# Performance work log

Hardware: AMD Instinct MI355X
Metric: run time of the kernel (lower is better)

Reference implementation:

```python
import jax, jax.numpy as jnp
import numpy as np

DIM = 1024
HEADS = 16
DIM_HEAD = 64
INNER = HEADS * DIM_HEAD  # 1024
MLP = 4096
EPS = 1e-5


def layer_norm(x, gamma, beta):
    mu = jnp.mean(x, axis=-1, keepdims=True)
    var = jnp.var(x, axis=-1, keepdims=True)
    return (x - mu) * jax.lax.rsqrt(var + EPS) * gamma + beta


def setup_inputs() -> dict:
    key = jax.random.key(0)
    ks = jax.random.split(key, 10)
    s = 0.02
    return {
        "x": jax.random.normal(ks[0], (2, 2048, DIM), dtype=jnp.float32),
        "ln1_g": jnp.ones((DIM,), jnp.float32),
        "ln1_b": jnp.zeros((DIM,), jnp.float32),
        "w_qkv": jax.random.normal(ks[1], (DIM, 3 * INNER), jnp.float32) * s,
        "w_out": jax.random.normal(ks[2], (INNER, DIM), jnp.float32) * s,
        "b_out": jnp.zeros((DIM,), jnp.float32),
        "ln2_g": jnp.ones((DIM,), jnp.float32),
        "ln2_b": jnp.zeros((DIM,), jnp.float32),
        "w1": jax.random.normal(ks[3], (DIM, MLP), jnp.float32) * s,
        "b1": jnp.zeros((MLP,), jnp.float32),
        "w2": jax.random.normal(ks[4], (MLP, DIM), jnp.float32) * s,
        "b2": jnp.zeros((DIM,), jnp.float32),
    }


def reference(x, ln1_g, ln1_b, w_qkv, w_out, b_out, ln2_g, ln2_b, w1, b1, w2, b2):
    b, n, _ = x.shape
    scale = DIM_HEAD ** -0.5

    # --- attention sublayer (pre-norm) ---
    h = layer_norm(x, ln1_g, ln1_b)
    qkv = h @ w_qkv  # [b, n, 3*inner]
    q, k, v = jnp.split(qkv, 3, axis=-1)
    # [b, n, inner] -> [b, heads, n, dim_head]
    def to_heads(t):
        return t.reshape(b, n, HEADS, DIM_HEAD).transpose(0, 2, 1, 3)
    q, k, v = to_heads(q), to_heads(k), to_heads(v)
    dots = jnp.einsum('bhid,bhjd->bhij', q, k) * scale  # [b,h,n,n]
    attn = jax.nn.softmax(dots, axis=-1)
    out = jnp.einsum('bhij,bhjd->bhid', attn, v)
    out = out.transpose(0, 2, 1, 3).reshape(b, n, INNER)
    x = out @ w_out + b_out + x

    # --- FFN sublayer (pre-norm) ---
    h = layer_norm(x, ln2_g, ln2_b)
    h = jax.nn.gelu(h @ w1 + b1, approximate=False)
    x = h @ w2 + b2 + x
    return x
```

## Files before the change

kernel.cpp:

```cpp
#include <hip/hip_runtime.h>
#include <hip/hip_bf16.h>
#include <math.h>

#define SEQ 2048
#define BATCH 2
#define TOKENS 4096
#define HEADS 16
#define DHEAD 64
#define TOKSTRIDE 3072

typedef __attribute__((ext_vector_type(4))) float f32x4;
typedef __attribute__((ext_vector_type(16))) float f32x16;
typedef __attribute__((ext_vector_type(8))) __bf16 bf16x8;
typedef __attribute__((ext_vector_type(8))) unsigned short ushort8;
typedef __attribute__((ext_vector_type(4))) unsigned short ushort4_t;
typedef __attribute__((ext_vector_type(4))) unsigned u32x4;
typedef __attribute__((ext_vector_type(2))) unsigned u32x2;

#if __has_builtin(__builtin_amdgcn_exp2f)
#define EXP2(x) __builtin_amdgcn_exp2f(x)
#else
#define EXP2(x) exp2f(x)
#endif

#if __has_builtin(__builtin_amdgcn_permlane32_swap)
#define HAS_PL32 1
#else
#define HAS_PL32 0
#endif

__device__ __forceinline__ unsigned short f2bf(float f) {
  unsigned u = __builtin_bit_cast(unsigned, f);
  u += 0x7fffu + ((u >> 16) & 1u);
  return (unsigned short)(u >> 16);
}

__device__ __forceinline__ float bf2f(unsigned short s) {
  unsigned u = ((unsigned)s) << 16;
  return __builtin_bit_cast(float, u);
}

__device__ __forceinline__ unsigned cvt_pk_bf16(float lo, float hi) {
  unsigned r;
  asm("v_cvt_pk_bf16_f32 %0, %1, %2" : "=v"(r) : "v"(lo), "v"(hi));
  return r;
}

__device__ __forceinline__ void cp16(const void* g, void* l) {
  __builtin_amdgcn_global_load_lds((const __attribute__((address_space(1))) void*)g,
                                   (__attribute__((address_space(3))) void*)l, 16, 0, 0);
}

#define FENCE asm volatile("" ::: "memory")
#define BARR  do { FENCE; __builtin_amdgcn_s_barrier(); FENCE; } while (0)

__global__ __launch_bounds__(256) void ln_rows(const float* __restrict__ x,
                                               const float* __restrict__ g,
                                               const float* __restrict__ b,
                                               unsigned short* __restrict__ out) {
  const int row = blockIdx.x;
  const int t = threadIdx.x;
  const f32x4* x4 = (const f32x4*)(x + (size_t)row * 1024);
  f32x4 v = x4[t];
  float sum = v[0] + v[1] + v[2] + v[3];
  float ss  = v[0]*v[0] + v[1]*v[1] + v[2]*v[2] + v[3]*v[3];
#pragma unroll
  for (int off = 1; off < 64; off <<= 1) {
    sum += __shfl_xor(sum, off);
    ss  += __shfl_xor(ss, off);
  }
  __shared__ float red[8];
  const int w = t >> 6, l = t & 63;
  if (l == 0) { red[w] = sum; red[w + 4] = ss; }
  __syncthreads();
  sum = red[0] + red[1] + red[2] + red[3];
  ss  = red[4] + red[5] + red[6] + red[7];
  const float mean = sum * (1.0f / 1024.0f);
  const float var  = ss * (1.0f / 1024.0f) - mean * mean;
  const float rs = rsqrtf(var + 1e-5f);
  ushort4_t o;
#pragma unroll
  for (int j = 0; j < 4; ++j) {
    float gv = g[t * 4 + j], bv = b[t * 4 + j];
    o[j] = f2bf((v[j] - mean) * rs * gv + bv);
  }
  *(ushort4_t*)(out + (size_t)row * 1024 + t * 4) = o;
}

__global__ __launch_bounds__(256) void ln_rows_bf(const unsigned short* __restrict__ x,
                                                  const float* __restrict__ g,
                                                  const float* __restrict__ b,
                                                  unsigned short* __restrict__ out) {
  const int row = blockIdx.x;
  const int t = threadIdx.x;
  ushort4_t v4 = *(const ushort4_t*)(x + (size_t)row * 1024 + t * 4);
  float v[4] = {bf2f(v4[0]), bf2f(v4[1]), bf2f(v4[2]), bf2f(v4[3])};
  float sum = v[0] + v[1] + v[2] + v[3];
  float ss  = v[0]*v[0] + v[1]*v[1] + v[2]*v[2] + v[3]*v[3];
#pragma unroll
  for (int off = 1; off < 64; off <<= 1) {
    sum += __shfl_xor(sum, off);
    ss  += __shfl_xor(ss, off);
  }
  __shared__ float red[8];
  const int w = t >> 6, l = t & 63;
  if (l == 0) { red[w] = sum; red[w + 4] = ss; }
  __syncthreads();
  sum = red[0] + red[1] + red[2] + red[3];
  ss  = red[4] + red[5] + red[6] + red[7];
  const float mean = sum * (1.0f / 1024.0f);
  const float var  = ss * (1.0f / 1024.0f) - mean * mean;
  const float rs = rsqrtf(var + 1e-5f);
  ushort4_t o;
#pragma unroll
  for (int j = 0; j < 4; ++j) {
    float gv = g[t * 4 + j], bv = b[t * 4 + j];
    o[j] = f2bf((v[j] - mean) * rs * gv + bv);
  }
  *(ushort4_t*)(out + (size_t)row * 1024 + t * 4) = o;
}

__global__ __launch_bounds__(256) void transpose_cast(const float* __restrict__ w,
                                                      unsigned short* __restrict__ wt,
                                                      int K, int N, float scale, int nscaled) {
  __shared__ float tile[32][33];
  const int n0 = blockIdx.x * 32, k0 = blockIdx.y * 32;
  const int tx = threadIdx.x & 31;
  const int ty = threadIdx.x >> 5;
#pragma unroll
  for (int i = 0; i < 4; ++i)
    tile[ty + 8 * i][tx] = w[(size_t)(k0 + ty + 8 * i) * N + n0 + tx];
  __syncthreads();
#pragma unroll
  for (int i = 0; i < 4; ++i) {
    int n = n0 + ty + 8 * i;
    float s = (n < nscaled) ? scale : 1.0f;
    wt[(size_t)n * K + k0 + tx] = f2bf(tile[tx][ty + 8 * i] * s);
  }
}

template <int EPI, int BN, int MINW, int NSPLIT>
__global__ __launch_bounds__(256, MINW) void gemm_bt(
    const unsigned short* __restrict__ A, const unsigned short* __restrict__ Bt,
    void* __restrict__ Cp, const float* __restrict__ bias, const void* __restrict__ resv,
    int M, int N, int K) {
  constexpr int BM = 128, BK = 64;
  constexpr int MR = BM / 32, NR = BN / 32;
  constexpr int AIT = BM * BK / 2048;
  constexpr int BIT = BN * BK / 2048;
  __shared__ unsigned short la[BM * BK];
  __shared__ unsigned short lb[BN * BK];
  const int t = threadIdx.x;
  const int w = t >> 6, l = t & 63;
  const int nwg = gridDim.x;
  const int bid = blockIdx.x;
  const int bid2 = (bid & 7) * (nwg >> 3) + (bid >> 3);
  const int nmn = nwg / NSPLIT;
  const int ksl = bid2 / nmn;
  const int rmn = bid2 - ksl * nmn;
  const int nx = N / BN;
  const int m0 = (rmn / nx) * BM, n0 = (rmn % nx) * BN;
  const int klen = K / NSPLIT;
  const int kbeg = ksl * klen;
  const int wr = w >> 1, wc = w & 1;
  const int lrow = l & 15, lk4 = l >> 4;
  f32x4 acc[MR][NR] = {};

  for (int k0 = kbeg; k0 < kbeg + klen; k0 += BK) {
#pragma unroll
    for (int i = 0; i < AIT; ++i) {
      int idx = t + 256 * i;
      int row = idx >> 3, seg = idx & 7;
      int ss = seg ^ (row & 7);
      cp16(A + (size_t)(m0 + row) * K + k0 + ss * 8, (char*)la + w * 1024 + i * 4096);
    }
#pragma unroll
    for (int i = 0; i < BIT; ++i) {
      int idx = t + 256 * i;
      int row = idx >> 3, seg = idx & 7;
      int ss = seg ^ (row & 7);
      cp16(Bt + (size_t)(n0 + row) * K + k0 + ss * 8, (char*)lb + w * 1024 + i * 4096);
    }
    __syncthreads();
#pragma unroll
    for (int ks = 0; ks < 2; ++ks) {
      bf16x8 af[MR], bfr[NR];
#pragma unroll
      for (int mi = 0; mi < MR; ++mi) {
        int row = wr * (BM / 2) + mi * 16 + lrow;
        int ss = (ks * 4 + lk4) ^ (row & 7);
        af[mi] = *(const bf16x8*)((const char*)la + row * 128 + ss * 16);
      }
#pragma unroll
      for (int ni = 0; ni < NR; ++ni) {
        int row = wc * (BN / 2) + ni * 16 + lrow;
        int ss = (ks * 4 + lk4) ^ (row & 7);
        bfr[ni] = *(const bf16x8*)((const char*)lb + row * 128 + ss * 16);
      }
#pragma unroll
      for (int mi = 0; mi < MR; ++mi)
#pragma unroll
        for (int ni = 0; ni < NR; ++ni)
          acc[mi][ni] = __builtin_amdgcn_mfma_f32_16x16x32_bf16(af[mi], bfr[ni], acc[mi][ni], 0, 0, 0);
    }
    __syncthreads();
  }

#pragma unroll
  for (int mi = 0; mi < MR; ++mi) {
    int rowb = m0 + wr * (BM / 2) + mi * 16 + lk4 * 4;
#pragma unroll
    for (int ni = 0; ni < NR; ++ni) {
      int col = n0 + wc * (BN / 2) + ni * 16 + lrow;
      f32x4 a = acc[mi][ni];
#pragma unroll
      for (int r = 0; r < 4; ++r) {
        size_t off = (size_t)(rowb + r) * N + col;
        if (EPI == 0) {
          ((unsigned short*)Cp)[off] = f2bf(a[r]);
        } else if (EPI == 2) {
          float v = a[r] + bias[col];
          ((unsigned short*)Cp)[off] = f2bf(0.5f * v * (1.0f + erff(v * 0.70710678f)));
        } else if (EPI == 3) {
          ((unsigned short*)Cp)[off] = f2bf(a[r] + bias[col] + ((const float*)resv)[off]);
        } else if (EPI == 4) {
          ((float*)Cp)[off] = a[r] + bias[col] + bf2f(((const unsigned short*)resv)[off]);
        } else {
          ((unsigned short*)Cp)[(size_t)ksl * M * N + off] = f2bf(a[r]);
        }
      }
    }
  }
}

__global__ __launch_bounds__(256) void mlp2_combine(const unsigned short* __restrict__ p,
                                                    const float* __restrict__ b2,
                                                    const unsigned short* __restrict__ xa,
                                                    float* __restrict__ out) {
  const int row = blockIdx.x, t = threadIdx.x;
  const size_t off = (size_t)row * 1024 + t * 4;
  ushort4_t a = *(const ushort4_t*)(p + off);
  ushort4_t b = *(const ushort4_t*)(p + (size_t)TOKENS * 1024 + off);
  f32x4 bb = *(const f32x4*)(b2 + t * 4);
  ushort4_t xv = *(const ushort4_t*)(xa + off);
  f32x4 o;
#pragma unroll
  for (int j = 0; j < 4; ++j) o[j] = bf2f(a[j]) + bf2f(b[j]) + bb[j] + bf2f(xv[j]);
  *(f32x4*)(out + off) = o;
}

__global__ __launch_bounds__(256, 2) void attn4(const unsigned short* __restrict__ qkv,
                                                unsigned short* __restrict__ Op,
                                                float2* __restrict__ ml) {
  __shared__ unsigned short lk_[64 * 64];
  __shared__ unsigned short lvt[64 * 64];
  const int t = threadIdx.x, wv = t >> 6, l = t & 63;
  const int chunk = blockIdx.x & 3, qb = blockIdx.x >> 2;
  const int h = blockIdx.y, b = blockIdx.z;
  const size_t tok0 = (size_t)b * SEQ;
  const int lq = l & 31, hi = l >> 5, l7 = l & 7;
  const int qrow = qb * 128 + wv * 32 + lq;
  const int kstart = chunk * 8;

  bf16x8 qf[4];
#pragma unroll
  for (int dc = 0; dc < 4; ++dc)
    qf[dc] = *(const bf16x8*)(qkv + (tok0 + qrow) * TOKSTRIDE + h * DHEAD + dc * 16 + hi * 8);

  float mrun = -1e30f, lsum = 0.0f;
  f32x16 o0 = {}, o1 = {};

  {
#pragma unroll
    for (int i = 0; i < 2; ++i) {
      int idx = t + 256 * i;
      int key = idx >> 3, seg = idx & 7;
      cp16(qkv + (tok0 + kstart * 64 + key) * TOKSTRIDE + 1024 + h * DHEAD + ((seg ^ (key & 7)) << 3),
           (char*)lk_ + wv * 1024 + i * 4096);
    }
#pragma unroll
    for (int i = 0; i < 2; ++i) {
      int idx = t + 256 * i;
      int key = idx & 63, seg = idx >> 6;
      ushort8 v8 = *(const ushort8*)(qkv + (tok0 + kstart * 64 + key) * TOKSTRIDE + 2048 + h * DHEAD + seg * 8);
#pragma unroll
      for (int j = 0; j < 8; ++j) {
        int d = seg * 8 + j;
        lvt[d * 64 + (((key >> 3) ^ (d & 7)) << 3) + (key & 7)] = v8[j];
      }
    }
  }
  __syncthreads();

  for (int kb = 0; kb < 8; ++kb) {
    const bool more = (kb + 1 < 8);
    const int kpre = kstart + kb + 1;

    f32x16 s0 = {}, s1 = {};
    __builtin_amdgcn_s_setprio(1);
#pragma unroll
    for (int dc = 0; dc < 4; ++dc) {
      int sgA = (dc * 2 + hi) ^ l7;
      bf16x8 kf0 = *(const bf16x8*)((const char*)lk_ + lq * 128 + (sgA << 4));
      bf16x8 kf1 = *(const bf16x8*)((const char*)lk_ + (32 + lq) * 128 + (sgA << 4));
      s0 = __builtin_amdgcn_mfma_f32_32x32x16_bf16(kf0, qf[dc], s0, 0, 0, 0);
      s1 = __builtin_amdgcn_mfma_f32_32x32x16_bf16(kf1, qf[dc], s1, 0, 0, 0);
    }
    __builtin_amdgcn_s_setprio(0);

    asm volatile("s_waitcnt lgkmcnt(0)" ::: "memory");
    BARR;
    __builtin_amdgcn_sched_barrier(0);

    ushort8 vpre[2];
    if (more) {
#pragma unroll
      for (int i = 0; i < 2; ++i) {
        int idx = t + 256 * i;
        int key = idx >> 3, seg = idx & 7;
        cp16(qkv + (tok0 + kpre * 64 + key) * TOKSTRIDE + 1024 + h * DHEAD + ((seg ^ (key & 7)) << 3),
             (char*)lk_ + wv * 1024 + i * 4096);
      }
#pragma unroll
      for (int i = 0; i < 2; ++i) {
        int idx = t + 256 * i;
        int key = idx & 63, seg = idx >> 6;
        vpre[i] = *(const ushort8*)(qkv + (tok0 + kpre * 64 + key) * TOKSTRIDE + 2048 + h * DHEAD + seg * 8);
      }
    }

    float mx[8];
#pragma unroll
    for (int r = 0; r < 8; ++r)
      mx[r] = fmaxf(fmaxf(s0[r], s0[r + 8]), fmaxf(s1[r], s1[r + 8]));
#pragma unroll
    for (int r = 0; r < 4; ++r) mx[r] = fmaxf(mx[r], mx[r + 4]);
    float m01 = fmaxf(fmaxf(mx[0], mx[1]), fmaxf(mx[2], mx[3]));
    float pm = fmaxf(m01, __shfl_xor(m01, 32));

    if (__any(pm > mrun + 8.0f)) {
      float mn = fmaxf(mrun, pm);
      float alpha = EXP2(mrun - mn);
      mrun = mn;
      lsum *= alpha;
#pragma unroll
      for (int r = 0; r < 16; ++r) {
        int qi = (r & 3) + 8 * (r >> 2) + 4 * hi;
        float ar = __shfl(alpha, qi);
        o0[r] *= ar; o1[r] *= ar;
      }
    }

    float p0[16], p1[16], ts[16];
#pragma unroll
    for (int r = 0; r < 16; ++r) { p0[r] = EXP2(s0[r] - mrun); }
#pragma unroll
    for (int r = 0; r < 16; ++r) { p1[r] = EXP2(s1[r] - mrun); }
#pragma unroll
    for (int r = 0; r < 16; ++r) ts[r] = p0[r] + p1[r];
#pragma unroll
    for (int st = 8; st > 0; st >>= 1)
#pragma unroll
      for (int r = 0; r < 8; ++r)
        if (r < st) ts[r] += ts[r + st];
    float psum = ts[0] + __shfl_xor(ts[0], 32);
    lsum += psum;

    unsigned W0[8], W1[8];
#pragma unroll
    for (int mI = 0; mI < 8; ++mI) {
      W0[mI] = cvt_pk_bf16(p0[2 * mI], p0[2 * mI + 1]);
      W1[mI] = cvt_pk_bf16(p1[2 * mI], p1[2 * mI + 1]);
    }
#if !HAS_PL32
    unsigned X0[8], X1[8];
#pragma unroll
    for (int mI = 0; mI < 8; ++mI) {
      X0[mI] = __shfl_xor((int)W0[mI], 32);
      X1[mI] = __shfl_xor((int)W1[mI], 32);
    }
#endif

    __builtin_amdgcn_s_setprio(1);
#pragma unroll
    for (int kt = 0; kt < 2; ++kt) {
#pragma unroll
      for (int c = 0; c < 2; ++c) {
        u32x4 fw;
#if HAS_PL32
        unsigned a0 = (kt == 0) ? W0[4 * c + 0] : W1[4 * c + 0];
        unsigned a1 = (kt == 0) ? W0[4 * c + 1] : W1[4 * c + 1];
        unsigned b0 = (kt == 0) ? W0[4 * c + 2] : W1[4 * c + 2];
        unsigned b1 = (kt == 0) ? W0[4 * c + 3] : W1[4 * c + 3];
        u32x2 pa = __builtin_amdgcn_permlane32_swap(a0, b0, false, false);
        u32x2 pb = __builtin_amdgcn_permlane32_swap(a1, b1, false, false);
        fw[0] = pa[0]; fw[1] = pb[0]; fw[2] = pa[1]; fw[3] = pb[1];
#else
        if (kt == 0) {
          fw[0] = hi ? X0[4 * c + 2] : W0[4 * c + 0];
          fw[1] = hi ? X0[4 * c + 3] : W0[4 * c + 1];
          fw[2] = hi ? W0[4 * c + 2] : X0[4 * c + 0];
          fw[3] = hi ? W0[4 * c + 3] : X0[4 * c + 1];
        } else {
          fw[0] = hi ? X1[4 * c + 2] : W1[4 * c + 0];
          fw[1] = hi ? X1[4 * c + 3] : W1[4 * c + 1];
          fw[2] = hi ? W1[4 * c + 2] : X1[4 * c + 0];
          fw[3] = hi ? W1[4 * c + 3] : X1[4 * c + 1];
        }
#endif
        bf16x8 pf = __builtin_bit_cast(bf16x8, fw);
        int ksg = (kt * 4 + c * 2 + hi) ^ l7;
        bf16x8 vfA = *(const bf16x8*)((const char*)lvt + lq * 128 + (ksg << 4));
        bf16x8 vfB = *(const bf16x8*)((const char*)lvt + (32 + lq) * 128 + (ksg << 4));
        o0 = __builtin_amdgcn_mfma_f32_32x32x16_bf16(pf, vfA, o0, 0, 0, 0);
        o1 = __builtin_amdgcn_mfma_f32_32x32x16_bf16(pf, vfB, o1, 0, 0, 0);
      }
    }
    __builtin_amdgcn_s_setprio(0);

    asm volatile("s_waitcnt lgkmcnt(0)" ::: "memory");
    BARR;
    __builtin_amdgcn_sched_barrier(0);

    if (more) {
#pragma unroll
      for (int i = 0; i < 2; ++i) {
        int idx = t + 256 * i;
        int key = idx & 63, seg = idx >> 6;
#pragma unroll
        for (int j = 0; j < 8; ++j) {
          int d = seg * 8 + j;
          lvt[d * 64 + (((key >> 3) ^ (d & 7)) << 3) + (key & 7)] = vpre[i][j];
        }
      }
    }
    asm volatile("s_waitcnt vmcnt(0) lgkmcnt(0)" ::: "memory");
    BARR;
    __builtin_amdgcn_sched_barrier(0);
  }

  const size_t cbase = (size_t)chunk * TOKENS;
#pragma unroll
  for (int r = 0; r < 16; ++r) {
    int qi = (r & 3) + 8 * (r >> 2) + 4 * hi;
    size_t rowoff = (cbase + tok0 + qb * 128 + wv * 32 + qi) * (size_t)1024 + h * DHEAD;
    Op[rowoff + lq]      = f2bf(o0[r]);
    Op[rowoff + 32 + lq] = f2bf(o1[r]);
  }
  if (l < 32) {
    size_t tokr = tok0 + qb * 128 + wv * 32 + lq;
    ml[(cbase + tokr) * 16 + h] = make_float2(mrun, lsum);
  }
}

__global__ __launch_bounds__(256) void attn_combine4(const unsigned short* __restrict__ Op,
                                                     const float2* __restrict__ ml,
                                                     unsigned short* __restrict__ out) {
  const int t = threadIdx.x, w = t >> 6, l = t & 63;
  const size_t tok = blockIdx.x * 4 + w;
#pragma unroll
  for (int h = 0; h < 16; ++h) {
    float2 mm[4];
#pragma unroll
    for (int c = 0; c < 4; ++c) mm[c] = ml[((size_t)c * TOKENS + tok) * 16 + h];
    float M = fmaxf(fmaxf(mm[0].x, mm[1].x), fmaxf(mm[2].x, mm[3].x));
    float wgt[4];
    float den = 0.0f;
#pragma unroll
    for (int c = 0; c < 4; ++c) { wgt[c] = EXP2(mm[c].x - M); den += mm[c].y * wgt[c]; }
    float inv = 1.0f / den;
    int col = h * 64 + l;
    float o = 0.0f;
#pragma unroll
    for (int c = 0; c < 4; ++c)
      o += bf2f(Op[((size_t)c * TOKENS + tok) * 1024 + col]) * wgt[c];
    out[tok * 1024 + col] = f2bf(o * inv);
  }
}

extern "C" void kernel_launch(void* const* d_in, const int* in_sizes, int n_in,
                              void* d_out, int out_size, void* d_ws, size_t ws_size,
                              hipStream_t stream) {
  const float* x    = (const float*)d_in[0];
  const float* ln1g = (const float*)d_in[1];
  const float* ln1b = (const float*)d_in[2];
  const float* wqkv = (const float*)d_in[3];
  const float* wout = (const float*)d_in[4];
  const float* bout = (const float*)d_in[5];
  const float* ln2g = (const float*)d_in[6];
  const float* ln2b = (const float*)d_in[7];
  const float* w1   = (const float*)d_in[8];
  const float* b1   = (const float*)d_in[9];
  const float* w2   = (const float*)d_in[10];
  const float* b2   = (const float*)d_in[11];

  char* ws = (char*)d_ws;
  unsigned short* wqkvT = (unsigned short*)ws; ws += (size_t)3072 * 1024 * 2;
  unsigned short* woutT = (unsigned short*)ws; ws += (size_t)1024 * 1024 * 2;
  unsigned short* w1T   = (unsigned short*)ws; ws += (size_t)4096 * 1024 * 2;
  unsigned short* w2T   = (unsigned short*)ws; ws += (size_t)1024 * 4096 * 2;
  unsigned short* h1    = (unsigned short*)ws; ws += (size_t)TOKENS * 1024 * 2;
  unsigned short* qkvb  = (unsigned short*)ws; ws += (size_t)TOKENS * 3072 * 2;
  unsigned short* attno = (unsigned short*)ws; ws += (size_t)TOKENS * 1024 * 2;
  unsigned short* xa    = (unsigned short*)ws; ws += (size_t)TOKENS * 1024 * 4;
  unsigned short* h2    = (unsigned short*)ws; ws += (size_t)TOKENS * 1024 * 2;
  unsigned short* hid   = (unsigned short*)ws; ws += (size_t)TOKENS * 4096 * 2;
  float2*         mlbuf = (float2*)ws;         ws += (size_t)4 * TOKENS * 16 * 8;
  unsigned short* Opart = hid;
  unsigned short* mlp2p = h1;

  transpose_cast<<<dim3(3072 / 32, 1024 / 32), 256, 0, stream>>>(wqkv, wqkvT, 1024, 3072, 0.18033688f, 1024);
  transpose_cast<<<dim3(1024 / 32, 1024 / 32), 256, 0, stream>>>(wout, woutT, 1024, 1024, 1.0f, 0);
  transpose_cast<<<dim3(4096 / 32, 1024 / 32), 256, 0, stream>>>(w1, w1T, 1024, 4096, 1.0f, 0);
  transpose_cast<<<dim3(1024 / 32, 4096 / 32), 256, 0, stream>>>(w2, w2T, 4096, 1024, 1.0f, 0);

  ln_rows<<<TOKENS, 256, 0, stream>>>(x, ln1g, ln1b, h1);
  gemm_bt<0, 128, 2, 1><<<768, 256, 0, stream>>>(h1, wqkvT, qkvb, nullptr, nullptr, TOKENS, 3072, 1024);
  attn4<<<dim3(4 * SEQ / 128, HEADS, BATCH), 256, 0, stream>>>(qkvb, Opart, mlbuf);
  attn_combine4<<<TOKENS / 4, 256, 0, stream>>>(Opart, mlbuf, attno);
  gemm_bt<3, 64, 3, 1><<<512, 256, 0, stream>>>(attno, woutT, xa, bout, x, TOKENS, 1024, 1024);
  ln_rows_bf<<<TOKENS, 256, 0, stream>>>(xa, ln2g, ln2b, h2);
  gemm_bt<2, 128, 2, 1><<<1024, 256, 0, stream>>>(h2, w1T, hid, b1, nullptr, TOKENS, 4096, 1024);
  gemm_bt<5, 128, 2, 2><<<512, 256, 0, stream>>>(hid, w2T, mlp2p, nullptr, nullptr, TOKENS, 1024, 4096);
  mlp2_combine<<<TOKENS, 256, 0, stream>>>(mlp2p, b2, xa, (float*)d_out);
}
```

Baseline: 240.5 us.

## Fuse split-KV attention combine into output projection GEMM; merge weight transposes

Removes the standalone attention-combine kernel. The output-projection GEMM now merges the four split-KV partial outputs (using the stored max and sum values) while it loads its A tile, so the combined attention output never goes to memory. It also merges the four weight transpose-cast launches into one launch that picks its matrix by block index. The trade-off is that each projection block recomputes the combine for its A rows once per N tile. The A loads also become synchronous register loads in place of async copies, which may reduce overlap.

```diff
diff --git a/kernel.cpp b/kernel.cpp
--- a/kernel.cpp
+++ b/kernel.cpp
@@ -120,11 +120,20 @@
   *(ushort4_t*)(out + (size_t)row * 1024 + t * 4) = o;
 }
 
-__global__ __launch_bounds__(256) void transpose_cast(const float* __restrict__ w,
-                                                      unsigned short* __restrict__ wt,
-                                                      int K, int N, float scale, int nscaled) {
+__global__ __launch_bounds__(256) void transpose_all(
+    const float* __restrict__ wqkv, const float* __restrict__ wout,
+    const float* __restrict__ w1, const float* __restrict__ w2,
+    unsigned short* __restrict__ wqkvT, unsigned short* __restrict__ woutT,
+    unsigned short* __restrict__ w1T, unsigned short* __restrict__ w2T) {
   __shared__ float tile[32][33];
-  const int n0 = blockIdx.x * 32, k0 = blockIdx.y * 32;
+  const int bid = blockIdx.x;
+  const float* w; unsigned short* wt; int K, N, lb; float scale; int nscaled;
+  if (bid < 3072)      { w = wqkv; wt = wqkvT; K = 1024; N = 3072; lb = bid;        scale = 0.18033688f; nscaled = 1024; }
+  else if (bid < 4096) { w = wout; wt = woutT; K = 1024; N = 1024; lb = bid - 3072; scale = 1.0f; nscaled = 0; }
+  else if (bid < 8192) { w = w1;   wt = w1T;   K = 1024; N = 4096; lb = bid - 4096; scale = 1.0f; nscaled = 0; }
+  else                 { w = w2;   wt = w2T;   K = 4096; N = 1024; lb = bid - 8192; scale = 1.0f; nscaled = 0; }
+  const int nx = N / 32;
+  const int n0 = (lb % nx) * 32, k0 = (lb / nx) * 32;
   const int tx = threadIdx.x & 31;
   const int ty = threadIdx.x >> 5;
 #pragma unroll
@@ -221,13 +230,108 @@
         } else if (EPI == 2) {
           float v = a[r] + bias[col];
           ((unsigned short*)Cp)[off] = f2bf(0.5f * v * (1.0f + erff(v * 0.70710678f)));
-        } else if (EPI == 3) {
-          ((unsigned short*)Cp)[off] = f2bf(a[r] + bias[col] + ((const float*)resv)[off]);
         } else if (EPI == 4) {
           ((float*)Cp)[off] = a[r] + bias[col] + bf2f(((const unsigned short*)resv)[off]);
         } else {
           ((unsigned short*)Cp)[(size_t)ksl * M * N + off] = f2bf(a[r]);
         }
+      }
+    }
+  }
+}
+
+__global__ __launch_bounds__(256, 3) void proj_fused(
+    const unsigned short* __restrict__ Op, const float2* __restrict__ ml,
+    const unsigned short* __restrict__ Bt, unsigned short* __restrict__ Cp,
+    const float* __restrict__ bias, const float* __restrict__ res,
+    int M, int N, int K) {
+  constexpr int BM = 128, BN = 64, BK = 64;
+  constexpr int MR = 4, NR = 2;
+  constexpr int BIT = 2;
+  __shared__ unsigned short la[BM * BK];
+  __shared__ unsigned short lb[BN * BK];
+  const int t = threadIdx.x;
+  const int w = t >> 6, l = t & 63;
+  const int nwg = gridDim.x;
+  const int bid = blockIdx.x;
+  const int bid2 = (bid & 7) * (nwg >> 3) + (bid >> 3);
+  const int nx = N / BN;
+  const int m0 = (bid2 / nx) * BM, n0 = (bid2 % nx) * BN;
+  const int wr = w >> 1, wc = w & 1;
+  const int lrow = l & 15, lk4 = l >> 4;
+  f32x4 acc[MR][NR] = {};
+
+  for (int k0 = 0; k0 < K; k0 += BK) {
+    const int h = k0 >> 6;
+#pragma unroll
+    for (int i = 0; i < BIT; ++i) {
+      int idx = t + 256 * i;
+      int row = idx >> 3, seg = idx & 7;
+      int ss = seg ^ (row & 7);
+      cp16(Bt + (size_t)(n0 + row) * K + k0 + ss * 8, (char*)lb + w * 1024 + i * 4096);
+    }
+#pragma unroll
+    for (int i = 0; i < 4; ++i) {
+      int idx = t + 256 * i;
+      int row = idx >> 3, seg = idx & 7;
+      int grow = m0 + row;
+      float2 mm[4];
+#pragma unroll
+      for (int c = 0; c < 4; ++c) mm[c] = ml[((size_t)c * TOKENS + grow) * 16 + h];
+      float Mx = fmaxf(fmaxf(mm[0].x, mm[1].x), fmaxf(mm[2].x, mm[3].x));
+      float wgt[4], den = 0.0f;
+#pragma unroll
+      for (int c = 0; c < 4; ++c) { wgt[c] = EXP2(mm[c].x - Mx); den += mm[c].y * wgt[c]; }
+      float inv = 1.0f / den;
+      ushort8 op[4];
+#pragma unroll
+      for (int c = 0; c < 4; ++c)
+        op[c] = *(const ushort8*)(Op + ((size_t)c * TOKENS + grow) * 1024 + h * 64 + seg * 8);
+      ushort8 o8;
+#pragma unroll
+      for (int j = 0; j < 8; ++j) {
+        float v = wgt[0] * bf2f(op[0][j]) + wgt[1] * bf2f(op[1][j]) +
+                  wgt[2] * bf2f(op[2][j]) + wgt[3] * bf2f(op[3][j]);
+        o8[j] = f2bf(v * inv);
+      }
+      *(ushort8*)((char*)la + row * 128 + ((seg ^ (row & 7)) << 4)) = o8;
+    }
+    __syncthreads();
+#pragma unroll
+    for (int ks = 0; ks < 2; ++ks) {
+      bf16x8 af[MR], bfr[NR];
+#pragma unroll
+      for (int mi = 0; mi < MR; ++mi) {
+        int row = wr * (BM / 2) + mi * 16 + lrow;
+        int ss = (ks * 4 + lk4) ^ (row & 7);
+        af[mi] = *(const bf16x8*)((const char*)la + row * 128 + ss * 16);
+      }
+#pragma unroll
+      for (int ni = 0; ni < NR; ++ni) {
+        int row = wc * (BN / 2) + ni * 16 + lrow;
+        int ss = (ks * 4 + lk4) ^ (row & 7);
+        bfr[ni] = *(const bf16x8*)((const char*)lb + row * 128 + ss * 16);
+      }
+#pragma unroll
+      for (int mi = 0; mi < MR; ++mi)
+#pragma unroll
+        for (int ni = 0; ni < NR; ++ni)
+          acc[mi][ni] = __builtin_amdgcn_mfma_f32_16x16x32_bf16(af[mi], bfr[ni], acc[mi][ni], 0, 0, 0);
+    }
+    __syncthreads();
+  }
+
+#pragma unroll
+  for (int mi = 0; mi < MR; ++mi) {
+    int rowb = m0 + wr * (BM / 2) + mi * 16 + lk4 * 4;
+#pragma unroll
+    for (int ni = 0; ni < NR; ++ni) {
+      int col = n0 + wc * (BN / 2) + ni * 16 + lrow;
+      f32x4 a = acc[mi][ni];
+#pragma unroll
+      for (int r = 0; r < 4; ++r) {
+        size_t off = (size_t)(rowb + r) * N + col;
+        Cp[off] = f2bf(a[r] + bias[col] + res[off]);
       }
     }
   }
@@ -453,31 +557,6 @@
   }
 }
 
-__global__ __launch_bounds__(256) void attn_combine4(const unsigned short* __restrict__ Op,
-                                                     const float2* __restrict__ ml,
-                                                     unsigned short* __restrict__ out) {
-  const int t = threadIdx.x, w = t >> 6, l = t & 63;
-  const size_t tok = blockIdx.x * 4 + w;
-#pragma unroll
-  for (int h = 0; h < 16; ++h) {
-    float2 mm[4];
-#pragma unroll
-    for (int c = 0; c < 4; ++c) mm[c] = ml[((size_t)c * TOKENS + tok) * 16 + h];
-    float M = fmaxf(fmaxf(mm[0].x, mm[1].x), fmaxf(mm[2].x, mm[3].x));
-    float wgt[4];
-    float den = 0.0f;
-#pragma unroll
-    for (int c = 0; c < 4; ++c) { wgt[c] = EXP2(mm[c].x - M); den += mm[c].y * wgt[c]; }
-    float inv = 1.0f / den;
-    int col = h * 64 + l;
-    float o = 0.0f;
-#pragma unroll
-    for (int c = 0; c < 4; ++c)
-      o += bf2f(Op[((size_t)c * TOKENS + tok) * 1024 + col]) * wgt[c];
-    out[tok * 1024 + col] = f2bf(o * inv);
-  }
-}
-
 extern "C" void kernel_launch(void* const* d_in, const int* in_sizes, int n_in,
                               void* d_out, int out_size, void* d_ws, size_t ws_size,
                               hipStream_t stream) {
@@ -509,16 +588,12 @@
   unsigned short* Opart = hid;
   unsigned short* mlp2p = h1;
 
-  transpose_cast<<<dim3(3072 / 32, 1024 / 32), 256, 0, stream>>>(wqkv, wqkvT, 1024, 3072, 0.18033688f, 1024);
-  transpose_cast<<<dim3(1024 / 32, 1024 / 32), 256, 0, stream>>>(wout, woutT, 1024, 1024, 1.0f, 0);
-  transpose_cast<<<dim3(4096 / 32, 1024 / 32), 256, 0, stream>>>(w1, w1T, 1024, 4096, 1.0f, 0);
-  transpose_cast<<<dim3(1024 / 32, 4096 / 32), 256, 0, stream>>>(w2, w2T, 4096, 1024, 1.0f, 0);
+  transpose_all<<<12288, 256, 0, stream>>>(wqkv, wout, w1, w2, wqkvT, woutT, w1T, w2T);
 
   ln_rows<<<TOKENS, 256, 0, stream>>>(x, ln1g, ln1b, h1);
   gemm_bt<0, 128, 2, 1><<<768, 256, 0, stream>>>(h1, wqkvT, qkvb, nullptr, nullptr, TOKENS, 3072, 1024);
   attn4<<<dim3(4 * SEQ / 128, HEADS, BATCH), 256, 0, stream>>>(qkvb, Opart, mlbuf);
-  attn_combine4<<<TOKENS / 4, 256, 0, stream>>>(Opart, mlbuf, attno);
-  gemm_bt<3, 64, 3, 1><<<512, 256, 0, stream>>>(attno, woutT, xa, bout, x, TOKENS, 1024, 1024);
+  proj_fused<<<512, 256, 0, stream>>>(Opart, mlbuf, woutT, xa, bout, x, TOKENS, 1024, 1024);
   ln_rows_bf<<<TOKENS, 256, 0, stream>>>(xa, ln2g, ln2b, h2);
   gemm_bt<2, 128, 2, 1><<<1024, 256, 0, stream>>>(h2, w1T, hid, b1, nullptr, TOKENS, 4096, 1024);
   gemm_bt<5, 128, 2, 2><<<512, 256, 0, stream>>>(hid, w2T, mlp2p, nullptr, nullptr, TOKENS, 1024, 4096);
```

After: 264.2 us. +9.9%, slower.
